# Kernel tuning notes

Measured on AMD Instinct MI355X. Metric: run time of the kernel, lower is better.

## Reference

```python
import jax, jax.numpy as jnp
import numpy as np

T, BS, N = 256, 512, 2048
FUDGE = 1e-4


def setup_inputs() -> dict:
    key = jax.random.key(0)
    ks = jax.random.split(key, 6)
    f32 = jnp.float32
    return {
        "noises": jax.random.normal(ks[0], (T, BS), f32) * 0.1,  # per-step process noise [T, bs]
        "ys": jax.random.normal(ks[1], (T,), f32),               # per-step scalar targets
        "qs": jax.random.normal(ks[2], (T,), f32),               # per-step scalar context input
        "z_biases": jax.random.normal(ks[3], (N,), f32),         # random-feature bias directions
        "w_in": jax.random.normal(ks[4], (N,), f32),             # random input weights
        "w_inq": jax.random.normal(ks[5], (N,), f32),            # random q-input weights
        # scalar learned params (legacy init values)
        "log_learning_rate": jnp.array(-6.0, f32),
        "log_learning_rate_decay": jnp.array(0.0, f32),
        "sigma_b": jnp.array(0.1, f32),
        "output_scale": jnp.array(1.0, f32),
        "u_feedback_scale": jnp.array(1.0, f32),
        "log_weight_decay": jnp.array(-0.001, f32),
        "q_scale": jnp.array(1.0, f32),
        "tauqlpf_m1": jnp.array(-1.0, f32),
        "tauylpf_m1": jnp.array(-1.0, f32),
    }


def _forward(noises, ys, qs, z_biases, w_in, w_inq,
             log_learning_rate, log_learning_rate_decay, sigma_b,
             output_scale, u_feedback_scale, log_weight_decay, q_scale,
             tauqlpf_m1, tauylpf_m1):
    bs = noises.shape[1]
    n = w_in.shape[0]
    softplus = lambda v: jnp.log1p(jnp.exp(v))
    biases = sigma_b * z_biases                    # [n]
    lr0 = jnp.exp(log_learning_rate)               # scalar
    tauq = 1.0 + softplus(tauqlpf_m1)
    tauy = 1.0 + softplus(tauylpf_m1)
    wd = jnp.exp(log_weight_decay)                 # tie_lr_weight_decay=False -> scalar decay
    lr_decay_rate = jnp.exp(log_learning_rate_decay)

    def step(carry, inp):
        w_out, u, e, lr_mult, qlp, ylp = carry
        y, noise_x, q = inp
        qlp = (1.0 - tauq) * qlp + tauq * q
        q_in = w_inq * (q_scale * qlp)             # [n]
        x = u * u_feedback_scale + e + noise_x     # noise injected at node 'x'; [bs]
        h = jax.nn.relu(biases[None, :] + x[:, None] * w_in[None, :] + q_in[None, :])  # [bs, n]
        u = jnp.einsum('kj,kj->k', w_out, h)       # [bs]
        a_mean = output_scale * u                  # [bs]
        # y observed every step (no None/NaN branch)
        ylp = (1.0 - tauy) * ylp + tauy * y
        e = ylp - u                                # [bs]
        lr = lr0 * lr_mult                         # [bs]
        dw = e[:, None] * h * lr[:, None]          # [bs, n]
        w_out = w_out + dw
        norms = jnp.sqrt(FUDGE + jnp.sum(dw * dw, axis=1))
        lr_mult = lr_mult * jnp.exp(-lr_decay_rate * norms)
        w_out = wd * w_out
        return (w_out, u, e, lr_mult, qlp, ylp), a_mean

    init = (jnp.zeros((bs, n), noises.dtype),
            jnp.zeros((bs,), noises.dtype),
            jnp.zeros((bs,), noises.dtype),
            jnp.ones((bs,), noises.dtype),
            jnp.zeros((), noises.dtype),
            jnp.zeros((), noises.dtype))
    _, a_means = jax.lax.scan(step, init, (ys, noises, qs))
    return a_means  # [T, bs]


def reference(noises, ys, qs, z_biases, w_in, w_inq,
              log_learning_rate, log_learning_rate_decay, sigma_b,
              output_scale, u_feedback_scale, log_weight_decay, q_scale,
              tauqlpf_m1, tauylpf_m1):
    return _forward(noises, ys, qs, z_biases, w_in, w_inq,
                    log_learning_rate, log_learning_rate_decay, sigma_b,
                    output_scale, u_feedback_scale, log_weight_decay, q_scale,
                    tauqlpf_m1, tauylpf_m1)
```

## Files before the change

kernel.cpp:

```cpp
#include <hip/hip_runtime.h>
#include <math.h>

#define T_STEPS 256
#define BS      512
#define N       2048
#define WAVE    64
#define EPT     (N / WAVE)
#define NCHUNK  (EPT / 4)
#define FUDGE   1e-4f

template <int CTRL>
__device__ __forceinline__ float dpp_add(float v) {
    int sh = __builtin_amdgcn_update_dpp(0, __float_as_int(v), CTRL, 0xf, 0xf, true);
    return v + __int_as_float(sh);
}

__device__ __forceinline__ float wave_allsum(float v) {
    v = dpp_add<0x111>(v);
    v = dpp_add<0x112>(v);
    v = dpp_add<0x114>(v);
    v = dpp_add<0x118>(v);
    v = dpp_add<0x142>(v);
    v = dpp_add<0x143>(v);
    return __int_as_float(__builtin_amdgcn_readlane(__float_as_int(v), 63));
}

__global__ __attribute__((amdgpu_waves_per_eu(1, 1))) __launch_bounds__(WAVE)
void legacy_elbo_scan_kernel(
    const float* __restrict__ noises,
    const float* __restrict__ ys,
    const float* __restrict__ qs,
    const float* __restrict__ z_biases,
    const float* __restrict__ w_in,
    const float* __restrict__ w_inq,
    const float* __restrict__ p_llr,
    const float* __restrict__ p_llrd,
    const float* __restrict__ p_sigb,
    const float* __restrict__ p_oscale,
    const float* __restrict__ p_ufs,
    const float* __restrict__ p_lwd,
    const float* __restrict__ p_qscale,
    const float* __restrict__ p_tauq,
    const float* __restrict__ p_tauy,
    float* __restrict__ out)
{
    const int lane = threadIdx.x;
    const int blk  = blockIdx.x;

    __shared__ float4 cb[N / 4];
    __shared__ float4 cw[N / 4];
    __shared__ float4 cq[N / 4];
    __shared__ float  ys_s[T_STEPS];
    __shared__ float  qs_s[T_STEPS];
    __shared__ float  nz_s[T_STEPS];

    const float sigb = p_sigb[0];

    const float4* zb4 = (const float4*)z_biases;
    const float4* wi4 = (const float4*)w_in;
    const float4* wq4 = (const float4*)w_inq;
#pragma unroll
    for (int i = 0; i < NCHUNK; ++i) {
        const int idx = lane + (i << 6);
        float4 b = zb4[idx];
        b.x *= sigb; b.y *= sigb; b.z *= sigb; b.w *= sigb;
        cb[idx] = b;
        cw[idx] = wi4[idx];
        cq[idx] = wq4[idx];
    }
#pragma unroll
    for (int i = 0; i < T_STEPS / WAVE; ++i) {
        const int t = lane + (i << 6);
        ys_s[t] = ys[t];
        qs_s[t] = qs[t];
        nz_s[t] = noises[t * BS + blk];
    }

    const float llr     = p_llr[0];
    const float llrd    = p_llrd[0];
    const float oscale  = p_oscale[0];
    const float ufs     = p_ufs[0];
    const float lwd     = p_lwd[0];
    const float qscale  = p_qscale[0];
    const float tauq_m1 = p_tauq[0];
    const float tauy_m1 = p_tauy[0];

    const float lr0      = expf(llr);
    const float lr_decay = expf(llrd);
    const float wd       = expf(lwd);
    const float rwd      = 1.0f / wd;
    const float tauq     = 1.0f + log1pf(expf(tauq_m1));
    const float tauy     = 1.0f + log1pf(expf(tauy_m1));
    const float omtq     = 1.0f - tauq;
    const float omty     = 1.0f - tauy;

    float v[EPT];
#pragma unroll
    for (int i = 0; i < EPT; ++i) v[i] = 0.0f;

    float u = 0.0f, e = 0.0f, lr_mult = 1.0f, qlp = 0.0f, ylp = 0.0f;
    float sp = 1.0f, rsp = 1.0f;

    __syncthreads();

    float q_c = qs_s[0], y_c = ys_s[0], n_c = nz_s[0];

    for (int t = 0; t < T_STEPS; ++t) {
        const int tn = (t + 1 < T_STEPS) ? t + 1 : t;
        const float q_n = qs_s[tn], y_n = ys_s[tn], n_n = nz_s[tn];

        qlp = omtq * qlp + tauq * q_c;
        const float qsc = qscale * qlp;
        const float x   = fmaf(u, ufs, e) + n_c;

        float su0 = 0.f, su1 = 0.f, sh0 = 0.f, sh1 = 0.f;
        float h[EPT];
#pragma unroll
        for (int c = 0; c < NCHUNK; ++c) {
            const int idx = lane + (c << 6);
            const float4 b4 = cb[idx];
            const float4 w4 = cw[idx];
            const float4 g4 = cq[idx];
            float h0 = fmaxf(fmaf(x, w4.x, fmaf(qsc, g4.x, b4.x)), 0.0f);
            float h1 = fmaxf(fmaf(x, w4.y, fmaf(qsc, g4.y, b4.y)), 0.0f);
            float h2 = fmaxf(fmaf(x, w4.z, fmaf(qsc, g4.z, b4.z)), 0.0f);
            float h3 = fmaxf(fmaf(x, w4.w, fmaf(qsc, g4.w, b4.w)), 0.0f);
            h[4*c+0] = h0; h[4*c+1] = h1; h[4*c+2] = h2; h[4*c+3] = h3;
            su0 = fmaf(v[4*c+0], h0, su0);
            su1 = fmaf(v[4*c+1], h1, su1);
            su0 = fmaf(v[4*c+2], h2, su0);
            su1 = fmaf(v[4*c+3], h3, su1);
            sh0 = fmaf(h0, h0, sh0);
            sh1 = fmaf(h1, h1, sh1);
            sh0 = fmaf(h2, h2, sh0);
            sh1 = fmaf(h3, h3, sh1);
        }
        const float su_t = wave_allsum(su0 + su1);
        const float sh2  = wave_allsum(sh0 + sh1);

        u = sp * su_t;
        if (lane == 0) out[t * BS + blk] = oscale * u;

        ylp = omty * ylp + tauy * y_c;
        e = ylp - u;
        const float el = e * (lr0 * lr_mult);
        const float c  = el * rsp;

#pragma unroll
        for (int i = 0; i < EPT; ++i)
            v[i] = fmaf(c, h[i], v[i]);

        const float nrm = sqrtf(fmaf(el * el, sh2, FUDGE));
        lr_mult *= expf(-lr_decay * nrm);
        sp  *= wd;
        rsp *= rwd;

        q_c = q_n; y_c = y_n; n_c = n_n;
    }
}

extern "C" void kernel_launch(void* const* d_in, const int* in_sizes, int n_in,
                              void* d_out, int out_size, void* d_ws, size_t ws_size,
                              hipStream_t stream) {
    (void)in_sizes; (void)n_in; (void)d_ws; (void)ws_size; (void)out_size;
    const float* noises   = (const float*)d_in[0];
    const float* ys       = (const float*)d_in[1];
    const float* qs       = (const float*)d_in[2];
    const float* z_biases = (const float*)d_in[3];
    const float* w_in     = (const float*)d_in[4];
    const float* w_inq    = (const float*)d_in[5];
    const float* llr      = (const float*)d_in[6];
    const float* llrd     = (const float*)d_in[7];
    const float* sigb     = (const float*)d_in[8];
    const float* oscale   = (const float*)d_in[9];
    const float* ufs      = (const float*)d_in[10];
    const float* lwd      = (const float*)d_in[11];
    const float* qscale   = (const float*)d_in[12];
    const float* tauq     = (const float*)d_in[13];
    const float* tauy     = (const float*)d_in[14];
    float* out = (float*)d_out;

    hipLaunchKernelGGL(legacy_elbo_scan_kernel, dim3(BS), dim3(WAVE), 0, stream,
                       noises, ys, qs, z_biases, w_in, w_inq,
                       llr, llrd, sigb, oscale, ufs, lwd, qscale, tauq, tauy,
                       out);
}
```

Measured before the change: 218.8 us.

## Split each batch row across four waves with LDS cross-wave reduction

Each block now has 256 threads (four waves) instead of a single wave. Each thread holds 8 weight elements instead of 32, and the per-step reductions combine per-wave DPP partials through a double-buffered shared array plus one barrier per step. The aim is to shorten the serial per-step dependency chain and cut register pressure, raising parallelism across the GPU. In exchange it adds a block-wide barrier and LDS traffic to every time step.

After: 213.2 us. 1.03x faster.

```diff
diff --git a/kernel.cpp b/kernel.cpp
--- a/kernel.cpp
+++ b/kernel.cpp
@@ -4,8 +4,9 @@
 #define T_STEPS 256
 #define BS      512
 #define N       2048
-#define WAVE    64
-#define EPT     (N / WAVE)
+#define BLOCK   256
+#define NWAVE   (BLOCK / 64)
+#define EPT     (N / BLOCK)
 #define NCHUNK  (EPT / 4)
 #define FUDGE   1e-4f
 
@@ -15,17 +16,17 @@
     return v + __int_as_float(sh);
 }
 
-__device__ __forceinline__ float wave_allsum(float v) {
+__device__ __forceinline__ float wave_sum_lane63(float v) {
     v = dpp_add<0x111>(v);
     v = dpp_add<0x112>(v);
     v = dpp_add<0x114>(v);
     v = dpp_add<0x118>(v);
     v = dpp_add<0x142>(v);
     v = dpp_add<0x143>(v);
-    return __int_as_float(__builtin_amdgcn_readlane(__float_as_int(v), 63));
+    return v;
 }
 
-__global__ __attribute__((amdgpu_waves_per_eu(1, 1))) __launch_bounds__(WAVE)
+__global__ __launch_bounds__(BLOCK)
 void legacy_elbo_scan_kernel(
     const float* __restrict__ noises,
     const float* __restrict__ ys,
@@ -44,7 +45,9 @@
     const float* __restrict__ p_tauy,
     float* __restrict__ out)
 {
-    const int lane = threadIdx.x;
+    const int tid  = threadIdx.x;
+    const int lane = tid & 63;
+    const int wid  = tid >> 6;
     const int blk  = blockIdx.x;
 
     __shared__ float4 cb[N / 4];
@@ -53,6 +56,7 @@
     __shared__ float  ys_s[T_STEPS];
     __shared__ float  qs_s[T_STEPS];
     __shared__ float  nz_s[T_STEPS];
+    __shared__ float  red[2][2 * NWAVE];
 
     const float sigb = p_sigb[0];
 
@@ -61,20 +65,16 @@
     const float4* wq4 = (const float4*)w_inq;
 #pragma unroll
     for (int i = 0; i < NCHUNK; ++i) {
-        const int idx = lane + (i << 6);
+        const int idx = tid + i * BLOCK;
         float4 b = zb4[idx];
         b.x *= sigb; b.y *= sigb; b.z *= sigb; b.w *= sigb;
         cb[idx] = b;
         cw[idx] = wi4[idx];
         cq[idx] = wq4[idx];
     }
-#pragma unroll
-    for (int i = 0; i < T_STEPS / WAVE; ++i) {
-        const int t = lane + (i << 6);
-        ys_s[t] = ys[t];
-        qs_s[t] = qs[t];
-        nz_s[t] = noises[t * BS + blk];
-    }
+    ys_s[tid] = ys[tid];
+    qs_s[tid] = qs[tid];
+    nz_s[tid] = noises[tid * BS + blk];
 
     const float llr     = p_llr[0];
     const float llrd    = p_llrd[0];
@@ -117,7 +117,7 @@
         float h[EPT];
 #pragma unroll
         for (int c = 0; c < NCHUNK; ++c) {
-            const int idx = lane + (c << 6);
+            const int idx = tid + c * BLOCK;
             const float4 b4 = cb[idx];
             const float4 w4 = cw[idx];
             const float4 g4 = cq[idx];
@@ -135,11 +135,22 @@
             sh0 = fmaf(h2, h2, sh0);
             sh1 = fmaf(h3, h3, sh1);
         }
-        const float su_t = wave_allsum(su0 + su1);
-        const float sh2  = wave_allsum(sh0 + sh1);
+        float su_w = wave_sum_lane63(su0 + su1);
+        float sh_w = wave_sum_lane63(sh0 + sh1);
+
+        const int p = t & 1;
+        if (lane == 63) {
+            red[p][wid * 2]     = su_w;
+            red[p][wid * 2 + 1] = sh_w;
+        }
+        __syncthreads();
+        const float4 r0 = *(const float4*)&red[p][0];
+        const float4 r1 = *(const float4*)&red[p][4];
+        const float su_t = (r0.x + r0.z) + (r1.x + r1.z);
+        const float sh2  = (r0.y + r0.w) + (r1.y + r1.w);
 
         u = sp * su_t;
-        if (lane == 0) out[t * BS + blk] = oscale * u;
+        if (tid == 0) out[t * BS + blk] = oscale * u;
 
         ylp = omty * ylp + tauy * y_c;
         e = ylp - u;
@@ -180,7 +191,7 @@
     const float* tauy     = (const float*)d_in[14];
     float* out = (float*)d_out;
 
-    hipLaunchKernelGGL(legacy_elbo_scan_kernel, dim3(BS), dim3(WAVE), 0, stream,
+    hipLaunchKernelGGL(legacy_elbo_scan_kernel, dim3(BS), dim3(BLOCK), 0, stream,
                        noises, ys, qs, z_biases, w_in, w_inq,
                        llr, llrd, sigb, oscale, ufs, lwd, qscale, tauq, tauy,
                        out);
```
